# Optimization experiments

Hardware: AMD Instinct MI355X
Metric: run time of the kernel (lower is better)

Reference implementation:

```python
import jax, jax.numpy as jnp
import numpy as np

KS = 7       # neighborhood kernel size (fixed in __init__)
HEADS = 8    # num_heads (fixed in __init__)
LN_EPS = 1e-5


def _nbr_idx(L, k):
    # NATTEN-style clamped window: window start shifts inward at borders (no padding)
    starts = jnp.clip(jnp.arange(L) - k // 2, 0, L - k)
    idx = starts[:, None] + jnp.arange(k)            # [L, k] absolute neighbor coords
    rel = idx - jnp.arange(L)[:, None] + (k - 1)     # [L, k] rel-pos-bias index in [0, 2k-2]
    return idx, rel


def _na2d(x, qkv_w, qkv_b, proj_w, proj_b, rpb):
    # x: [B, H, W, C]  -> neighborhood attention with clamped 7x7 windows
    B, H, W, C = x.shape
    hd = C // HEADS
    qkv = x @ qkv_w.T + qkv_b                        # [B,H,W,3C]
    q, k, v = jnp.split(qkv, 3, axis=-1)
    q = q.reshape(B, H, W, HEADS, hd) * (hd ** -0.5)
    k = k.reshape(B, H, W, HEADS, hd)
    v = v.reshape(B, H, W, HEADS, hd)
    ri, rri = _nbr_idx(H, KS)                        # [H,KS]
    ci, rci = _nbr_idx(W, KS)                        # [W,KS]
    # gather neighborhoods: [B,H,W,KS,KS,heads,hd]
    kn = k[:, ri[:, None, :, None], ci[None, :, None, :]]
    vn = v[:, ri[:, None, :, None], ci[None, :, None, :]]
    scores = jnp.einsum('bijhd,bijpqhd->bhijpq', q, kn)   # [B,heads,H,W,KS,KS]
    bias = rpb[:, rri[:, None, :, None], rci[None, :, None, :]]  # [heads,H,W,KS,KS]
    scores = scores + bias[None]
    attn = jax.nn.softmax(scores.reshape(B, HEADS, H, W, KS * KS), axis=-1)
    vn = vn.reshape(B, H, W, KS * KS, HEADS, hd)
    out = jnp.einsum('bhijp,bijphd->bijhd', attn, vn)      # [B,H,W,heads,hd]
    out = out.reshape(B, H, W, C)
    return out @ proj_w.T + proj_b


def _layernorm(x, g, b):
    mu = jnp.mean(x, axis=-1, keepdims=True)
    var = jnp.mean((x - mu) ** 2, axis=-1, keepdims=True)
    return (x - mu) * jax.lax.rsqrt(var + LN_EPS) * g + b


def setup_inputs() -> dict:
    key = jax.random.key(0)
    ks = jax.random.split(key, 4)
    B, T, H, W, C = 2, 8, 48, 48, 64
    return {
        'q': jax.random.normal(ks[0], (B, T, H, W, C), dtype=jnp.float32),
        'qkv_w': jax.random.normal(ks[1], (3 * C, C), dtype=jnp.float32) * 0.02,
        'qkv_b': jnp.zeros((3 * C,), jnp.float32),
        'proj_w': jax.random.normal(ks[2], (C, C), dtype=jnp.float32) * 0.02,
        'proj_b': jnp.zeros((C,), jnp.float32),
        'rpb': jax.random.normal(ks[3], (HEADS, 2 * KS - 1, 2 * KS - 1), dtype=jnp.float32) * 0.02,
        'ln_g': jnp.ones((C,), jnp.float32),
        'ln_b': jnp.zeros((C,), jnp.float32),
    }


def reference(q, qkv_w, qkv_b, proj_w, proj_b, rpb, ln_g, ln_b):
    B, T, H, W, C = q.shape
    x = q.reshape(B * T, H, W, C)                    # '(b t) h w c'
    x = _na2d(x, qkv_w, qkv_b, proj_w, proj_b, rpb)  # wPT path
    x = x.reshape(B, T, H, W, C)
    return _layernorm(x, ln_g, ln_b)                 # norm_q; wGC=False
```

## Files before the change

kernel.cpp:

```cpp
#include <hip/hip_runtime.h>
#include <hip/hip_bf16.h>

#define BT   16
#define IH   48
#define IW   48
#define CH   64
#define NH   8
#define HD   8
#define KS   7
#define NPIX (BT*IH*IW)
#define QKVC 192
#define LN_EPS 1e-5f
#define QSCALE 0.35355339059327373f

typedef __bf16 bf16_t;
typedef bf16_t bf16x8 __attribute__((ext_vector_type(8)));
typedef float  f32x4  __attribute__((ext_vector_type(4)));
typedef float  f32x2  __attribute__((ext_vector_type(2)));

__device__ __forceinline__ float bflo(unsigned u) { union { unsigned i; float f; } v; v.i = u << 16; return v.f; }
__device__ __forceinline__ float bfhi(unsigned u) { union { unsigned i; float f; } v; v.i = u & 0xffff0000u; return v.f; }
__device__ __forceinline__ f32x2 unp2(unsigned u) { f32x2 r; r.x = bflo(u); r.y = bfhi(u); return r; }

__device__ __forceinline__ bf16x8 pack_bf16x8(float4 lo, float4 hi) {
    bf16x8 r;
    r[0] = (bf16_t)lo.x; r[1] = (bf16_t)lo.y; r[2] = (bf16_t)lo.z; r[3] = (bf16_t)lo.w;
    r[4] = (bf16_t)hi.x; r[5] = (bf16_t)hi.y; r[6] = (bf16_t)hi.z; r[7] = (bf16_t)hi.w;
    return r;
}

__global__ __launch_bounds__(256) void qkv_kernel(
        const float* __restrict__ x,
        const float* __restrict__ w,
        const float* __restrict__ b,
        __hip_bfloat16* __restrict__ qkv) {
    const int gw   = blockIdx.x * 4 + (threadIdx.x >> 6);
    const int ngrp = gw % 3;
    const int mg   = gw / 3;
    const int l  = threadIdx.x & 63;
    const int m  = l & 15;
    const int kg = l >> 4;

    const int ch_base = ngrp * 64 + m * 4;
    const float4 bias4 = *(const float4*)(b + ch_base);
    const float scale = (ngrp == 0) ? QSCALE : 1.f;

    bf16x8 wb0[4], wb1[4];
    #pragma unroll
    for (int t = 0; t < 4; ++t) {
        const float* wr_ = w + (size_t)(ch_base + t) * CH + kg * 8;
        wb0[t] = pack_bf16x8(*(const float4*)(wr_),      *(const float4*)(wr_ + 4));
        wb1[t] = pack_bf16x8(*(const float4*)(wr_ + 32), *(const float4*)(wr_ + 36));
    }

    #pragma unroll
    for (int mm = 0; mm < 2; ++mm) {
        const int mtile = mg * 2 + mm;
        const float* xr = x + (size_t)(mtile * 16 + m) * CH + kg * 8;
        const bf16x8 a0 = pack_bf16x8(*(const float4*)(xr),      *(const float4*)(xr + 4));
        const bf16x8 a1 = pack_bf16x8(*(const float4*)(xr + 32), *(const float4*)(xr + 36));

        float val[4][4];
        #pragma unroll
        for (int t = 0; t < 4; ++t) {
            f32x4 acc = {0.f, 0.f, 0.f, 0.f};
            acc = __builtin_amdgcn_mfma_f32_16x16x32_bf16(a0, wb0[t], acc, 0, 0, 0);
            acc = __builtin_amdgcn_mfma_f32_16x16x32_bf16(a1, wb1[t], acc, 0, 0, 0);
            const float bias = (t == 0) ? bias4.x : (t == 1) ? bias4.y : (t == 2) ? bias4.z : bias4.w;
            #pragma unroll
            for (int r = 0; r < 4; ++r) val[t][r] = (acc[r] + bias) * scale;
        }
        #pragma unroll
        for (int r = 0; r < 4; ++r) {
            const int pix = mtile * 16 + kg * 4 + r;
            union { ushort4 u; __hip_bfloat16 hh[4]; } pk;
            #pragma unroll
            for (int t = 0; t < 4; ++t) pk.hh[t] = __float2bfloat16(val[t][r]);
            *reinterpret_cast<ushort4*>(qkv + (size_t)pix * QKVC + ch_base) = pk.u;
        }
    }
}

__global__ __launch_bounds__(256, 8) void attn_kernel(
        const __hip_bfloat16* __restrict__ qkv,
        const float* __restrict__ rpb,
        __hip_bfloat16* __restrict__ aout) {
    const int blk  = blockIdx.x;
    const int n    = blk & 15;
    const int tile = blk >> 4;
    const int i0   = (tile / 6) * 4;
    const int j0   = (tile % 6) * 8;
    const int tid  = threadIdx.x;
    const int h    = tid & 7;
    const int pl   = tid >> 3;
    const int i    = i0 + (pl >> 3);
    const int j    = j0 + (pl & 7);
    const size_t img = (size_t)n * (IH * IW);

    f32x2 qv[4];
    {
        const uint4 u = *reinterpret_cast<const uint4*>(
            qkv + (img + i * IW + j) * QKVC + h * HD);
        qv[0] = unp2(u.x); qv[1] = unp2(u.y); qv[2] = unp2(u.z); qv[3] = unp2(u.w);
    }

    int si = i - 3; si = si < 0 ? 0 : (si > IH - KS ? IH - KS : si);
    int sj = j - 3; sj = sj < 0 ? 0 : (sj > IW - KS ? IW - KS : sj);
    const float* rp = rpb + h * (2*KS-1) * (2*KS-1) + (sj - j + (KS - 1));

    float lrun = 0.f;
    f32x2 acc[4];
    #pragma unroll
    for (int d = 0; d < 4; ++d) acc[d] = (f32x2){0.f, 0.f};

    for (int p = 0; p < KS; ++p) {
        const int ki = si + p;
        const float* rprow = rp + (ki - i + (KS - 1)) * (2*KS-1);
        const __hip_bfloat16* row = qkv + (img + ki * IW + sj) * QKVC + CH + h * HD;

        uint4 kb[KS];
        float rb[KS];
        #pragma unroll
        for (int qq = 0; qq < KS; ++qq) {
            kb[qq] = *reinterpret_cast<const uint4*>(row + qq * QKVC);
            rb[qq] = rprow[qq];
        }
        float e[KS];
        #pragma unroll
        for (int qq = 0; qq < KS; ++qq) {
            f32x2 s2 = qv[0] * unp2(kb[qq].x);
            s2 += qv[1] * unp2(kb[qq].y);
            s2 += qv[2] * unp2(kb[qq].z);
            s2 += qv[3] * unp2(kb[qq].w);
            e[qq] = __expf(s2.x + s2.y + rb[qq]);
        }
        uint4 vb[KS];
        #pragma unroll
        for (int qq = 0; qq < KS; ++qq)
            vb[qq] = *reinterpret_cast<const uint4*>(row + qq * QKVC + CH);
        #pragma unroll
        for (int qq = 0; qq < KS; ++qq) {
            lrun += e[qq];
            acc[0] += e[qq] * unp2(vb[qq].x);
            acc[1] += e[qq] * unp2(vb[qq].y);
            acc[2] += e[qq] * unp2(vb[qq].z);
            acc[3] += e[qq] * unp2(vb[qq].w);
        }
    }
    const float inv = 1.f / lrun;
    union { uint4 u; __hip_bfloat16 hh[8]; } pk;
    #pragma unroll
    for (int d = 0; d < 4; ++d) {
        pk.hh[2*d]   = __float2bfloat16(acc[d].x * inv);
        pk.hh[2*d+1] = __float2bfloat16(acc[d].y * inv);
    }
    *reinterpret_cast<uint4*>(aout + (img + i * IW + j) * CH + h * HD) = pk.u;
}

__global__ __launch_bounds__(256) void proj_ln_kernel(
        const __hip_bfloat16* __restrict__ aout,
        const float* __restrict__ pw,
        const float* __restrict__ pb,
        const float* __restrict__ g,
        const float* __restrict__ beta,
        float* __restrict__ out) {
    const int mtile = (blockIdx.x * blockDim.x + threadIdx.x) >> 6;
    const int l  = threadIdx.x & 63;
    const int m  = l & 15;
    const int kg = l >> 4;

    const __hip_bfloat16* ar = aout + (size_t)(mtile * 16 + m) * CH + kg * 8;
    const bf16x8 a0 = *reinterpret_cast<const bf16x8*>(ar);
    const bf16x8 a1 = *reinterpret_cast<const bf16x8*>(ar + 32);

    const int ch_base = m * 4;
    const float4 bias4 = *(const float4*)(pb + ch_base);

    float val[4][4];
    #pragma unroll
    for (int t = 0; t < 4; ++t) {
        const float* wr_ = pw + (size_t)(ch_base + t) * CH + kg * 8;
        const bf16x8 b0 = pack_bf16x8(*(const float4*)(wr_),      *(const float4*)(wr_ + 4));
        const bf16x8 b1 = pack_bf16x8(*(const float4*)(wr_ + 32), *(const float4*)(wr_ + 36));
        f32x4 acc = {0.f, 0.f, 0.f, 0.f};
        acc = __builtin_amdgcn_mfma_f32_16x16x32_bf16(a0, b0, acc, 0, 0, 0);
        acc = __builtin_amdgcn_mfma_f32_16x16x32_bf16(a1, b1, acc, 0, 0, 0);
        const float bias = (t == 0) ? bias4.x : (t == 1) ? bias4.y : (t == 2) ? bias4.z : bias4.w;
        #pragma unroll
        for (int r = 0; r < 4; ++r) val[t][r] = acc[r] + bias;
    }

    float sm[4];
    #pragma unroll
    for (int r = 0; r < 4; ++r) sm[r] = val[0][r] + val[1][r] + val[2][r] + val[3][r];
    #pragma unroll
    for (int mask = 1; mask <= 8; mask <<= 1) {
        #pragma unroll
        for (int r = 0; r < 4; ++r) sm[r] += __shfl_xor(sm[r], mask, 64);
    }
    float mu[4];
    #pragma unroll
    for (int r = 0; r < 4; ++r) mu[r] = sm[r] * (1.f / 64.f);

    float qs[4];
    #pragma unroll
    for (int r = 0; r < 4; ++r) {
        float a = val[0][r] - mu[r], bq = val[1][r] - mu[r];
        float c = val[2][r] - mu[r], d = val[3][r] - mu[r];
        qs[r] = a * a + bq * bq + c * c + d * d;
    }
    #pragma unroll
    for (int mask = 1; mask <= 8; mask <<= 1) {
        #pragma unroll
        for (int r = 0; r < 4; ++r) qs[r] += __shfl_xor(qs[r], mask, 64);
    }
    float rs[4];
    #pragma unroll
    for (int r = 0; r < 4; ++r) rs[r] = rsqrtf(qs[r] * (1.f / 64.f) + LN_EPS);

    const float4 g4  = *(const float4*)(g + ch_base);
    const float4 be4 = *(const float4*)(beta + ch_base);
    #pragma unroll
    for (int r = 0; r < 4; ++r) {
        const int pix = mtile * 16 + kg * 4 + r;
        float4 o;
        o.x = (val[0][r] - mu[r]) * rs[r] * g4.x + be4.x;
        o.y = (val[1][r] - mu[r]) * rs[r] * g4.y + be4.y;
        o.z = (val[2][r] - mu[r]) * rs[r] * g4.z + be4.z;
        o.w = (val[3][r] - mu[r]) * rs[r] * g4.w + be4.w;
        *reinterpret_cast<float4*>(out + (size_t)pix * CH + ch_base) = o;
    }
}

extern "C" void kernel_launch(void* const* d_in, const int* in_sizes, int n_in,
                              void* d_out, int out_size, void* d_ws, size_t ws_size,
                              hipStream_t stream) {
    const float* x      = (const float*)d_in[0];
    const float* qkv_w  = (const float*)d_in[1];
    const float* qkv_b  = (const float*)d_in[2];
    const float* proj_w = (const float*)d_in[3];
    const float* proj_b = (const float*)d_in[4];
    const float* rpb    = (const float*)d_in[5];
    const float* ln_g   = (const float*)d_in[6];
    const float* ln_b   = (const float*)d_in[7];
    float* out = (float*)d_out;

    __hip_bfloat16* qkv  = (__hip_bfloat16*)d_ws;
    __hip_bfloat16* aout = (__hip_bfloat16*)((char*)d_ws + (size_t)NPIX * QKVC * 2);

    qkv_kernel<<<864, 256, 0, stream>>>(x, qkv_w, qkv_b, qkv);
    attn_kernel<<<1152, 256, 0, stream>>>(qkv, rpb, aout);
    proj_ln_kernel<<<576, 256, 0, stream>>>(aout, proj_w, proj_b, ln_g, ln_b, out);
}
```

Baseline: 120.8 us.

## Fuse neighborhood attention with output projection and layernorm via shared memory

Merges the attention kernel with the projection+LayerNorm kernel. Each block keeps its 32-pixel attention output in LDS and runs the MFMA projection and LayerNorm on two waves after a barrier. This removes the global round trip of the attention output and one kernel launch. In exchange only two of four waves do the epilogue, and the occupancy hint drops from 8 to 4 blocks per CU.

```diff
diff --git a/kernel.cpp b/kernel.cpp
--- a/kernel.cpp
+++ b/kernel.cpp
@@ -13,6 +13,11 @@
 #define LN_EPS 1e-5f
 #define QSCALE 0.35355339059327373f
 
+#define TSH  4
+#define TSW  8
+#define TP   (TSH*TSW)
+#define AOS  72
+
 typedef __bf16 bf16_t;
 typedef bf16_t bf16x8 __attribute__((ext_vector_type(8)));
 typedef float  f32x4  __attribute__((ext_vector_type(4)));
@@ -81,154 +86,159 @@
     }
 }
 
-__global__ __launch_bounds__(256, 8) void attn_kernel(
+__global__ __launch_bounds__(256, 4) void attn_proj_ln_kernel(
         const __hip_bfloat16* __restrict__ qkv,
         const float* __restrict__ rpb,
-        __hip_bfloat16* __restrict__ aout) {
-    const int blk  = blockIdx.x;
-    const int n    = blk & 15;
-    const int tile = blk >> 4;
-    const int i0   = (tile / 6) * 4;
-    const int j0   = (tile % 6) * 8;
-    const int tid  = threadIdx.x;
-    const int h    = tid & 7;
-    const int pl   = tid >> 3;
-    const int i    = i0 + (pl >> 3);
-    const int j    = j0 + (pl & 7);
-    const size_t img = (size_t)n * (IH * IW);
-
-    f32x2 qv[4];
-    {
-        const uint4 u = *reinterpret_cast<const uint4*>(
-            qkv + (img + i * IW + j) * QKVC + h * HD);
-        qv[0] = unp2(u.x); qv[1] = unp2(u.y); qv[2] = unp2(u.z); qv[3] = unp2(u.w);
-    }
-
-    int si = i - 3; si = si < 0 ? 0 : (si > IH - KS ? IH - KS : si);
-    int sj = j - 3; sj = sj < 0 ? 0 : (sj > IW - KS ? IW - KS : sj);
-    const float* rp = rpb + h * (2*KS-1) * (2*KS-1) + (sj - j + (KS - 1));
-
-    float lrun = 0.f;
-    f32x2 acc[4];
-    #pragma unroll
-    for (int d = 0; d < 4; ++d) acc[d] = (f32x2){0.f, 0.f};
-
-    for (int p = 0; p < KS; ++p) {
-        const int ki = si + p;
-        const float* rprow = rp + (ki - i + (KS - 1)) * (2*KS-1);
-        const __hip_bfloat16* row = qkv + (img + ki * IW + sj) * QKVC + CH + h * HD;
-
-        uint4 kb[KS];
-        float rb[KS];
-        #pragma unroll
-        for (int qq = 0; qq < KS; ++qq) {
-            kb[qq] = *reinterpret_cast<const uint4*>(row + qq * QKVC);
-            rb[qq] = rprow[qq];
-        }
-        float e[KS];
-        #pragma unroll
-        for (int qq = 0; qq < KS; ++qq) {
-            f32x2 s2 = qv[0] * unp2(kb[qq].x);
-            s2 += qv[1] * unp2(kb[qq].y);
-            s2 += qv[2] * unp2(kb[qq].z);
-            s2 += qv[3] * unp2(kb[qq].w);
-            e[qq] = __expf(s2.x + s2.y + rb[qq]);
-        }
-        uint4 vb[KS];
-        #pragma unroll
-        for (int qq = 0; qq < KS; ++qq)
-            vb[qq] = *reinterpret_cast<const uint4*>(row + qq * QKVC + CH);
-        #pragma unroll
-        for (int qq = 0; qq < KS; ++qq) {
-            lrun += e[qq];
-            acc[0] += e[qq] * unp2(vb[qq].x);
-            acc[1] += e[qq] * unp2(vb[qq].y);
-            acc[2] += e[qq] * unp2(vb[qq].z);
-            acc[3] += e[qq] * unp2(vb[qq].w);
-        }
-    }
-    const float inv = 1.f / lrun;
-    union { uint4 u; __hip_bfloat16 hh[8]; } pk;
-    #pragma unroll
-    for (int d = 0; d < 4; ++d) {
-        pk.hh[2*d]   = __float2bfloat16(acc[d].x * inv);
-        pk.hh[2*d+1] = __float2bfloat16(acc[d].y * inv);
-    }
-    *reinterpret_cast<uint4*>(aout + (img + i * IW + j) * CH + h * HD) = pk.u;
-}
-
-__global__ __launch_bounds__(256) void proj_ln_kernel(
-        const __hip_bfloat16* __restrict__ aout,
         const float* __restrict__ pw,
         const float* __restrict__ pb,
         const float* __restrict__ g,
         const float* __restrict__ beta,
         float* __restrict__ out) {
-    const int mtile = (blockIdx.x * blockDim.x + threadIdx.x) >> 6;
-    const int l  = threadIdx.x & 63;
-    const int m  = l & 15;
-    const int kg = l >> 4;
-
-    const __hip_bfloat16* ar = aout + (size_t)(mtile * 16 + m) * CH + kg * 8;
-    const bf16x8 a0 = *reinterpret_cast<const bf16x8*>(ar);
-    const bf16x8 a1 = *reinterpret_cast<const bf16x8*>(ar + 32);
-
-    const int ch_base = m * 4;
-    const float4 bias4 = *(const float4*)(pb + ch_base);
-
-    float val[4][4];
-    #pragma unroll
-    for (int t = 0; t < 4; ++t) {
-        const float* wr_ = pw + (size_t)(ch_base + t) * CH + kg * 8;
-        const bf16x8 b0 = pack_bf16x8(*(const float4*)(wr_),      *(const float4*)(wr_ + 4));
-        const bf16x8 b1 = pack_bf16x8(*(const float4*)(wr_ + 32), *(const float4*)(wr_ + 36));
-        f32x4 acc = {0.f, 0.f, 0.f, 0.f};
-        acc = __builtin_amdgcn_mfma_f32_16x16x32_bf16(a0, b0, acc, 0, 0, 0);
-        acc = __builtin_amdgcn_mfma_f32_16x16x32_bf16(a1, b1, acc, 0, 0, 0);
-        const float bias = (t == 0) ? bias4.x : (t == 1) ? bias4.y : (t == 2) ? bias4.z : bias4.w;
-        #pragma unroll
-        for (int r = 0; r < 4; ++r) val[t][r] = acc[r] + bias;
-    }
-
-    float sm[4];
-    #pragma unroll
-    for (int r = 0; r < 4; ++r) sm[r] = val[0][r] + val[1][r] + val[2][r] + val[3][r];
-    #pragma unroll
-    for (int mask = 1; mask <= 8; mask <<= 1) {
-        #pragma unroll
-        for (int r = 0; r < 4; ++r) sm[r] += __shfl_xor(sm[r], mask, 64);
-    }
-    float mu[4];
-    #pragma unroll
-    for (int r = 0; r < 4; ++r) mu[r] = sm[r] * (1.f / 64.f);
-
-    float qs[4];
-    #pragma unroll
-    for (int r = 0; r < 4; ++r) {
-        float a = val[0][r] - mu[r], bq = val[1][r] - mu[r];
-        float c = val[2][r] - mu[r], d = val[3][r] - mu[r];
-        qs[r] = a * a + bq * bq + c * c + d * d;
-    }
-    #pragma unroll
-    for (int mask = 1; mask <= 8; mask <<= 1) {
-        #pragma unroll
-        for (int r = 0; r < 4; ++r) qs[r] += __shfl_xor(qs[r], mask, 64);
-    }
-    float rs[4];
-    #pragma unroll
-    for (int r = 0; r < 4; ++r) rs[r] = rsqrtf(qs[r] * (1.f / 64.f) + LN_EPS);
-
-    const float4 g4  = *(const float4*)(g + ch_base);
-    const float4 be4 = *(const float4*)(beta + ch_base);
-    #pragma unroll
-    for (int r = 0; r < 4; ++r) {
-        const int pix = mtile * 16 + kg * 4 + r;
-        float4 o;
-        o.x = (val[0][r] - mu[r]) * rs[r] * g4.x + be4.x;
-        o.y = (val[1][r] - mu[r]) * rs[r] * g4.y + be4.y;
-        o.z = (val[2][r] - mu[r]) * rs[r] * g4.z + be4.z;
-        o.w = (val[3][r] - mu[r]) * rs[r] * g4.w + be4.w;
-        *reinterpret_cast<float4*>(out + (size_t)pix * CH + ch_base) = o;
+    __shared__ __align__(16) __hip_bfloat16 ao[TP * AOS];
+
+    const int blk  = blockIdx.x;
+    const int n    = blk & 15;
+    const int tile = blk >> 4;
+    const int i0   = (tile / 6) * TSH;
+    const int j0   = (tile % 6) * TSW;
+    const int tid  = threadIdx.x;
+    const size_t img = (size_t)n * (IH * IW);
+
+    {
+        const int h  = tid & 7;
+        const int pl = tid >> 3;
+        const int i  = i0 + (pl >> 3);
+        const int j  = j0 + (pl & 7);
+
+        f32x2 qv[4];
+        {
+            const uint4 u = *reinterpret_cast<const uint4*>(
+                qkv + (img + i * IW + j) * QKVC + h * HD);
+            qv[0] = unp2(u.x); qv[1] = unp2(u.y); qv[2] = unp2(u.z); qv[3] = unp2(u.w);
+        }
+
+        int si = i - 3; si = si < 0 ? 0 : (si > IH - KS ? IH - KS : si);
+        int sj = j - 3; sj = sj < 0 ? 0 : (sj > IW - KS ? IW - KS : sj);
+        const float* rp = rpb + h * (2*KS-1) * (2*KS-1) + (sj - j + (KS - 1));
+
+        float lrun = 0.f;
+        f32x2 acc[4];
+        #pragma unroll
+        for (int d = 0; d < 4; ++d) acc[d] = (f32x2){0.f, 0.f};
+
+        for (int p = 0; p < KS; ++p) {
+            const int ki = si + p;
+            const float* rprow = rp + (ki - i + (KS - 1)) * (2*KS-1);
+            const __hip_bfloat16* row = qkv + (img + ki * IW + sj) * QKVC + CH + h * HD;
+
+            uint4 kb[KS];
+            float rb[KS];
+            #pragma unroll
+            for (int qq = 0; qq < KS; ++qq) {
+                kb[qq] = *reinterpret_cast<const uint4*>(row + qq * QKVC);
+                rb[qq] = rprow[qq];
+            }
+            float e[KS];
+            #pragma unroll
+            for (int qq = 0; qq < KS; ++qq) {
+                f32x2 s2 = qv[0] * unp2(kb[qq].x);
+                s2 += qv[1] * unp2(kb[qq].y);
+                s2 += qv[2] * unp2(kb[qq].z);
+                s2 += qv[3] * unp2(kb[qq].w);
+                e[qq] = __expf(s2.x + s2.y + rb[qq]);
+            }
+            uint4 vb[KS];
+            #pragma unroll
+            for (int qq = 0; qq < KS; ++qq)
+                vb[qq] = *reinterpret_cast<const uint4*>(row + qq * QKVC + CH);
+            #pragma unroll
+            for (int qq = 0; qq < KS; ++qq) {
+                lrun += e[qq];
+                acc[0] += e[qq] * unp2(vb[qq].x);
+                acc[1] += e[qq] * unp2(vb[qq].y);
+                acc[2] += e[qq] * unp2(vb[qq].z);
+                acc[3] += e[qq] * unp2(vb[qq].w);
+            }
+        }
+        const float inv = 1.f / lrun;
+        union { uint4 u; __hip_bfloat16 hh[8]; } pk;
+        #pragma unroll
+        for (int d = 0; d < 4; ++d) {
+            pk.hh[2*d]   = __float2bfloat16(acc[d].x * inv);
+            pk.hh[2*d+1] = __float2bfloat16(acc[d].y * inv);
+        }
+        *reinterpret_cast<uint4*>(ao + pl * AOS + h * HD) = pk.u;
+    }
+    __syncthreads();
+
+    const int wv = tid >> 6;
+    if (wv < 2) {
+        const int l  = tid & 63;
+        const int m  = l & 15;
+        const int kg = l >> 4;
+
+        const __hip_bfloat16* ar = ao + (wv * 16 + m) * AOS + kg * 8;
+        const bf16x8 a0 = *reinterpret_cast<const bf16x8*>(ar);
+        const bf16x8 a1 = *reinterpret_cast<const bf16x8*>(ar + 32);
+
+        const int ch_base = m * 4;
+        const float4 bias4 = *(const float4*)(pb + ch_base);
+
+        float val[4][4];
+        #pragma unroll
+        for (int t = 0; t < 4; ++t) {
+            const float* wr_ = pw + (size_t)(ch_base + t) * CH + kg * 8;
+            const bf16x8 b0 = pack_bf16x8(*(const float4*)(wr_),      *(const float4*)(wr_ + 4));
+            const bf16x8 b1 = pack_bf16x8(*(const float4*)(wr_ + 32), *(const float4*)(wr_ + 36));
+            f32x4 acc = {0.f, 0.f, 0.f, 0.f};
+            acc = __builtin_amdgcn_mfma_f32_16x16x32_bf16(a0, b0, acc, 0, 0, 0);
+            acc = __builtin_amdgcn_mfma_f32_16x16x32_bf16(a1, b1, acc, 0, 0, 0);
+            const float bias = (t == 0) ? bias4.x : (t == 1) ? bias4.y : (t == 2) ? bias4.z : bias4.w;
+            #pragma unroll
+            for (int r = 0; r < 4; ++r) val[t][r] = acc[r] + bias;
+        }
+
+        float sm[4];
+        #pragma unroll
+        for (int r = 0; r < 4; ++r) sm[r] = val[0][r] + val[1][r] + val[2][r] + val[3][r];
+        #pragma unroll
+        for (int mask = 1; mask <= 8; mask <<= 1) {
+            #pragma unroll
+            for (int r = 0; r < 4; ++r) sm[r] += __shfl_xor(sm[r], mask, 64);
+        }
+        float mu[4];
+        #pragma unroll
+        for (int r = 0; r < 4; ++r) mu[r] = sm[r] * (1.f / 64.f);
+
+        float qs[4];
+        #pragma unroll
+        for (int r = 0; r < 4; ++r) {
+            float a = val[0][r] - mu[r], bq = val[1][r] - mu[r];
+            float c = val[2][r] - mu[r], d = val[3][r] - mu[r];
+            qs[r] = a * a + bq * bq + c * c + d * d;
+        }
+        #pragma unroll
+        for (int mask = 1; mask <= 8; mask <<= 1) {
+            #pragma unroll
+            for (int r = 0; r < 4; ++r) qs[r] += __shfl_xor(qs[r], mask, 64);
+        }
+        float rs[4];
+        #pragma unroll
+        for (int r = 0; r < 4; ++r) rs[r] = rsqrtf(qs[r] * (1.f / 64.f) + LN_EPS);
+
+        const float4 g4  = *(const float4*)(g + ch_base);
+        const float4 be4 = *(const float4*)(beta + ch_base);
+        #pragma unroll
+        for (int r = 0; r < 4; ++r) {
+            const int pl = wv * 16 + kg * 4 + r;
+            const int gi = i0 + (pl >> 3), gj = j0 + (pl & 7);
+            float4 o;
+            o.x = (val[0][r] - mu[r]) * rs[r] * g4.x + be4.x;
+            o.y = (val[1][r] - mu[r]) * rs[r] * g4.y + be4.y;
+            o.z = (val[2][r] - mu[r]) * rs[r] * g4.z + be4.z;
+            o.w = (val[3][r] - mu[r]) * rs[r] * g4.w + be4.w;
+            *reinterpret_cast<float4*>(out + (img + gi * IW + gj) * CH + ch_base) = o;
+        }
     }
 }
 
@@ -245,10 +255,9 @@
     const float* ln_b   = (const float*)d_in[7];
     float* out = (float*)d_out;
 
-    __hip_bfloat16* qkv  = (__hip_bfloat16*)d_ws;
-    __hip_bfloat16* aout = (__hip_bfloat16*)((char*)d_ws + (size_t)NPIX * QKVC * 2);
+    __hip_bfloat16* qkv = (__hip_bfloat16*)d_ws;
 
     qkv_kernel<<<864, 256, 0, stream>>>(x, qkv_w, qkv_b, qkv);
-    attn_kernel<<<1152, 256, 0, stream>>>(qkv, rpb, aout);
-    proj_ln_kernel<<<576, 256, 0, stream>>>(aout, proj_w, proj_b, ln_g, ln_b, out);
-}
+    attn_proj_ln_kernel<<<1152, 256, 0, stream>>>(qkv, rpb, proj_w, proj_b,
+                                                  ln_g, ln_b, out);
+}
```

Measured after the change: 115.8 us. 1.04x faster.
